# Performance work log

Hardware: AMD Instinct MI355X
Metric: run time of the kernel (lower is better)

Reference implementation:

```python
import jax, jax.numpy as jnp
import numpy as np
from jax import lax

NUM_TAGS = 9
HIDDEN = 768
BATCH = 64
SEQ = 512


def setup_inputs() -> dict:
    key = jax.random.key(0)
    ks = jax.random.split(key, 6)
    hidden = jax.random.normal(ks[0], (BATCH, SEQ, HIDDEN), dtype=jnp.float32)
    labels = jax.random.randint(ks[1], (BATCH, SEQ), 0, NUM_TAGS)  # all >= 0 -> full mask
    weight = jax.random.normal(ks[2], (NUM_TAGS, HIDDEN), dtype=jnp.float32) * 0.02
    bias = jnp.zeros((NUM_TAGS,), dtype=jnp.float32)
    start_transitions = jax.random.normal(ks[3], (NUM_TAGS,), dtype=jnp.float32) * 0.1
    end_transitions = jax.random.normal(ks[4], (NUM_TAGS,), dtype=jnp.float32) * 0.1
    transitions = jax.random.normal(ks[5], (NUM_TAGS, NUM_TAGS), dtype=jnp.float32) * 0.1
    return dict(hidden=hidden, labels=labels, weight=weight, bias=bias,
                start_transitions=start_transitions, end_transitions=end_transitions,
                transitions=transitions)


def _crf_log_likelihood(emissions, tags, mask, start_t, end_t, trans):
    """pytorch-crf log-likelihood, reduction='sum'.
    emissions [B,L,T] float, tags [B,L] int, mask [B,L] bool."""
    # --- numerator: score of the gold path ---
    tag0 = tags[:, 0]
    score0 = start_t[tag0] + jnp.take_along_axis(emissions[:, 0], tag0[:, None], axis=1)[:, 0]

    def num_step(carry, inp):
        score, prev = carry
        em, tg, m = inp  # em [B,T], tg [B], m [B]
        s = trans[prev, tg] + jnp.take_along_axis(em, tg[:, None], axis=1)[:, 0]
        score = score + jnp.where(m, s, jnp.zeros_like(s))
        prev = jnp.where(m, tg, prev)
        return (score, prev), None

    (num_score, last_tag), _ = lax.scan(
        num_step, (score0, tag0),
        (emissions[:, 1:].swapaxes(0, 1), tags[:, 1:].T, mask[:, 1:].T))
    numerator = num_score + end_t[last_tag]

    # --- denominator: forward algorithm (log-sum-exp recurrence) ---
    alpha0 = start_t[None, :] + emissions[:, 0]  # [B,T]

    def den_step(alpha, inp):
        em, m = inp  # em [B,T], m [B]
        nxt = jax.nn.logsumexp(alpha[:, :, None] + trans[None], axis=1) + em
        alpha = jnp.where(m[:, None], nxt, alpha)
        return alpha, None

    alpha, _ = lax.scan(den_step, alpha0,
                        (emissions[:, 1:].swapaxes(0, 1), mask[:, 1:].T))
    denominator = jax.nn.logsumexp(alpha + end_t[None, :], axis=1)

    return jnp.sum(numerator - denominator)


def _viterbi_decode(emissions, mask, start_t, end_t, trans):
    """Max-plus DP + backtrack. Returns padded [B,L] int32 best tag sequence."""
    B, L, T = emissions.shape
    score0 = start_t[None, :] + emissions[:, 0]  # [B,T]
    identity = jnp.arange(T, dtype=jnp.int32)[None, :]  # identity backpointer for masked steps

    def fwd_step(score, inp):
        em, m = inp  # em [B,T], m [B]
        br = score[:, :, None] + trans[None]  # [B,T_prev,T_cur]
        idx = jnp.argmax(br, axis=1).astype(jnp.int32)  # [B,T]
        nxt = jnp.max(br, axis=1) + em
        score = jnp.where(m[:, None], nxt, score)
        idx = jnp.where(m[:, None], idx, identity)
        return score, idx

    final, hist = lax.scan(fwd_step, score0,
                           (emissions[:, 1:].swapaxes(0, 1), mask[:, 1:].T))
    last_tag = jnp.argmax(final + end_t[None, :], axis=1).astype(jnp.int32)  # [B]

    def back_step(tag, idx):  # idx [B,T] backpointers for this position
        prev = jnp.take_along_axis(idx, tag[:, None], axis=1)[:, 0]
        return prev, tag

    first_tag, tags_rev = lax.scan(back_step, last_tag, hist, reverse=True)
    tags = jnp.concatenate([first_tag[None, :], tags_rev], axis=0).T  # [B,L]
    return tags * mask.astype(jnp.int32)


def reference(hidden, labels, weight, bias, start_transitions, end_transitions, transitions):
    mask_full = labels >= 0
    h = hidden[:, 1:-1, :]                       # drop [CLS]/[SEP] positions
    tags = labels[:, 1:-1] * mask_full[:, 1:-1]  # zero out padded labels
    mask = mask_full[:, 1:-1]
    # dropout is identity in eval mode
    emissions = jnp.einsum('blh,th->blt', h, weight) + bias  # [B,L,T]
    llh = _crf_log_likelihood(emissions, tags, mask,
                              start_transitions, end_transitions, transitions)
    tag_seqs = _viterbi_decode(emissions, mask,
                               start_transitions, end_transitions, transitions)
    return -llh, tag_seqs.astype(jnp.float32)
```

## Files before the change

kernel.cpp:

```cpp
#include <hip/hip_runtime.h>
#include <stdint.h>

#define NB 64
#define SEQL 512
#define L 510
#define T 9
#define H 768
#define EMS 12
#define LN2 0.6931471805599453f

__device__ __forceinline__ float rl(float v, int l) {
  return __uint_as_float(__builtin_amdgcn_readlane(__float_as_uint(v), l));
}

__global__ __launch_bounds__(256) void emis_kernel(
    const float* __restrict__ hidden, const float* __restrict__ weight,
    const float* __restrict__ bias, float* __restrict__ em,
    float* __restrict__ eem, float* __restrict__ out) {
  __shared__ float4 wl[T * 192];
  const float4* w4 = (const float4*)weight;
  for (int k = threadIdx.x; k < T * 192; k += 256) wl[k] = w4[k];
  if (blockIdx.x == 0 && threadIdx.x == 0) out[0] = 0.f;
  __syncthreads();
  const int lane = threadIdx.x & 63;
  const int wv = threadIdx.x >> 6;
  const int base = blockIdx.x * 64 + wv * 16;
#pragma unroll 1
  for (int pr = 0; pr < 8; ++pr) {
    const int r0 = base + pr * 2, r1 = r0 + 1;
    const int b0 = r0 / L, p0 = r0 - b0 * L;
    const int b1 = r1 / L, p1 = r1 - b1 * L;
    const float4* h0 = (const float4*)(hidden + ((size_t)(b0 * SEQL + p0 + 1)) * H);
    const float4* h1 = (const float4*)(hidden + ((size_t)(b1 * SEQL + p1 + 1)) * H);
    float4 ha[3], hb[3];
#pragma unroll
    for (int k = 0; k < 3; ++k) { ha[k] = h0[lane + 64 * k]; hb[k] = h1[lane + 64 * k]; }
    float a0[T], a1[T];
#pragma unroll
    for (int t = 0; t < T; ++t) { a0[t] = 0.f; a1[t] = 0.f; }
#pragma unroll
    for (int t = 0; t < T; ++t) {
#pragma unroll
      for (int k = 0; k < 3; ++k) {
        float4 w = wl[t * 192 + lane + 64 * k];
        a0[t] = fmaf(ha[k].x, w.x, fmaf(ha[k].y, w.y, fmaf(ha[k].z, w.z, fmaf(ha[k].w, w.w, a0[t]))));
        a1[t] = fmaf(hb[k].x, w.x, fmaf(hb[k].y, w.y, fmaf(hb[k].z, w.z, fmaf(hb[k].w, w.w, a1[t]))));
      }
    }
#pragma unroll
    for (int off = 32; off; off >>= 1) {
#pragma unroll
      for (int t = 0; t < T; ++t) {
        a0[t] += __shfl_xor(a0[t], off);
        a1[t] += __shfl_xor(a1[t], off);
      }
    }
    if (lane < 2) {
      const int rr = lane ? r1 : r0;
      float* eo = em + (size_t)rr * EMS;
      float* xo = eem + (size_t)rr * EMS;
#pragma unroll
      for (int t = 0; t < T; ++t) {
        float v = (lane ? a1[t] : a0[t]) + bias[t];
        eo[t] = v;
        xo[t] = __expf(v);
      }
    }
  }
}

__global__ __launch_bounds__(64) void chunk_kernel(
    const float* __restrict__ em, const float* __restrict__ eem,
    const float* __restrict__ trans, float* __restrict__ PdLn,
    float* __restrict__ Mv) {
  const int lane = threadIdx.x;
  const int m7 = lane / 9;
  const int i9 = lane - m7 * 9;
  const bool isden = blockIdx.x < 147;
  const int wid = isden ? blockIdx.x : blockIdx.x - 147;
  const int rtask = wid * 7 + (m7 < 7 ? m7 : 6);
  const bool act = (m7 < 7) && (rtask < 1024);
  const int task = act ? rtask : 0;
  const int b = task >> 4, s = task & 15;
  const int nt = (s == 15) ? 29 : 32;
  const int l0 = 32 * s + 1;

  if (isden) {
    float E[81];
#pragma unroll
    for (int k = 0; k < 81; ++k) E[k] = __expf(trans[k]);
    const float* ee = eem + ((size_t)(b * L + l0)) * EMS;
    float4 ea = *(const float4*)(ee);
    float4 eb = *(const float4*)(ee + 4);
    float e8 = ee[8];
    float ec[9] = {ea.x, ea.y, ea.z, ea.w, eb.x, eb.y, eb.z, eb.w, e8};
    float R[9];
#pragma unroll
    for (int j = 0; j < 9; ++j) R[j] = E[i9 * 9 + j] * ec[j];
    int iexp = 0;
    float4 na = *(const float4*)(ee + EMS);
    float4 nb = *(const float4*)(ee + EMS + 4);
    float n8 = ee[EMS + 8];
    for (int t = 1; t < nt; ++t) {
      float e0 = na.x, e1 = na.y, e2 = na.z, e3 = na.w;
      float e4 = nb.x, e5 = nb.y, e6 = nb.z, e7 = nb.w, e8c = n8;
      if (t < nt - 1) {
        na = *(const float4*)(ee + (size_t)(t + 1) * EMS);
        nb = *(const float4*)(ee + (size_t)(t + 1) * EMS + 4);
        n8 = ee[(size_t)(t + 1) * EMS + 8];
      }
      float Rn[9];
#pragma unroll
      for (int j = 0; j < 9; ++j) {
        float a = R[0] * E[0 * 9 + j];
#pragma unroll
        for (int k = 1; k < 9; ++k) a = fmaf(R[k], E[k * 9 + j], a);
        Rn[j] = a;
      }
      R[0] = Rn[0] * e0; R[1] = Rn[1] * e1; R[2] = Rn[2] * e2;
      R[3] = Rn[3] * e3; R[4] = Rn[4] * e4; R[5] = Rn[5] * e5;
      R[6] = Rn[6] * e6; R[7] = Rn[7] * e7; R[8] = Rn[8] * e8c;
      if ((t & 3) == 0) {
        float mx = R[0];
#pragma unroll
        for (int j = 1; j < 9; ++j) mx = fmaxf(mx, R[j]);
        int ex = (int)((__float_as_uint(mx) >> 23) & 0xff) - 127;
        iexp += ex;
        float sc = __uint_as_float((uint32_t)(127 - ex) << 23);
#pragma unroll
        for (int j = 0; j < 9; ++j) R[j] *= sc;
      }
    }
    if (act) {
      float ls = (float)iexp * LN2;
#pragma unroll
      for (int j = 0; j < 9; ++j)
        PdLn[(size_t)task * 81 + j * 9 + i9] = __logf(R[j]) + ls;
    }
  } else {
    float t_[81];
#pragma unroll
    for (int k = 0; k < 81; ++k) t_[k] = trans[k];
    const float* ep = em + ((size_t)(b * L + l0)) * EMS;
    float4 ea = *(const float4*)(ep);
    float4 eb = *(const float4*)(ep + 4);
    float e8 = ep[8];
    float ec[9] = {ea.x, ea.y, ea.z, ea.w, eb.x, eb.y, eb.z, eb.w, e8};
    float V[9];
#pragma unroll
    for (int j = 0; j < 9; ++j) V[j] = t_[i9 * 9 + j] + ec[j];
    float4 na = *(const float4*)(ep + EMS);
    float4 nb = *(const float4*)(ep + EMS + 4);
    float n8 = ep[EMS + 8];
    for (int t = 1; t < nt; ++t) {
      float e[9] = {na.x, na.y, na.z, na.w, nb.x, nb.y, nb.z, nb.w, n8};
      if (t < nt - 1) {
        na = *(const float4*)(ep + (size_t)(t + 1) * EMS);
        nb = *(const float4*)(ep + (size_t)(t + 1) * EMS + 4);
        n8 = ep[(size_t)(t + 1) * EMS + 8];
      }
      float Vn[9];
#pragma unroll
      for (int j = 0; j < 9; ++j) {
        float m = V[0] + t_[0 * 9 + j];
#pragma unroll
        for (int k = 1; k < 9; ++k) m = fmaxf(m, V[k] + t_[k * 9 + j]);
        Vn[j] = m + e[j];
      }
#pragma unroll
      for (int j = 0; j < 9; ++j) V[j] = Vn[j];
    }
    if (act) {
#pragma unroll
      for (int j = 0; j < 9; ++j)
        Mv[(size_t)task * 81 + j * 9 + i9] = V[j];
    }
  }
}

__global__ __launch_bounds__(64) void compose_kernel(
    const float* __restrict__ em, const int* __restrict__ labels,
    const float* __restrict__ PdLn, const float* __restrict__ Mv,
    const float* __restrict__ start_t, const float* __restrict__ end_t,
    const float* __restrict__ trans, unsigned char* __restrict__ chosen,
    float* __restrict__ out) {
  __shared__ float s_pd[16 * 81];
  __shared__ float s_mv[16 * 81];
  __shared__ float s_A[17 * 9];
  __shared__ float s_t[81];
  __shared__ int s_lab[L];
  const int b = blockIdx.x;
  const int lane = threadIdx.x;
  for (int k = lane; k < 16 * 81; k += 64) {
    s_pd[k] = PdLn[(size_t)b * 16 * 81 + k];
    s_mv[k] = Mv[(size_t)b * 16 * 81 + k];
  }
  for (int k = lane; k < 81; k += 64) s_t[k] = trans[k];
  for (int k = lane; k < L; k += 64) s_lab[k] = labels[b * SEQL + 1 + k];
  __syncthreads();

  const int jj = lane < 9 ? lane : 8;

  float part = 0.f;
  for (int l = lane; l < L; l += 64) {
    int tg = s_lab[l];
    float e = em[((size_t)(b * L + l)) * EMS + tg];
    if (l == 0) part += start_t[tg] + e;
    else part += s_t[s_lab[l - 1] * 9 + tg] + e;
    if (l == L - 1) part += end_t[tg];
  }
#pragma unroll
  for (int off = 32; off; off >>= 1) part += __shfl_xor(part, off);

  float D = start_t[jj] + em[(size_t)b * L * EMS + jj];
  for (int s = 0; s < 16; ++s) {
    const float* col = &s_pd[s * 81 + jj * 9];
    float v0 = rl(D, 0) + col[0], v1 = rl(D, 1) + col[1], v2 = rl(D, 2) + col[2];
    float v3 = rl(D, 3) + col[3], v4 = rl(D, 4) + col[4], v5 = rl(D, 5) + col[5];
    float v6 = rl(D, 6) + col[6], v7 = rl(D, 7) + col[7], v8 = rl(D, 8) + col[8];
    float mx = fmaxf(fmaxf(fmaxf(fmaxf(v0, v1), fmaxf(v2, v3)),
                           fmaxf(fmaxf(v4, v5), fmaxf(v6, v7))), v8);
    float sum = __expf(v0 - mx) + __expf(v1 - mx) + __expf(v2 - mx) +
                __expf(v3 - mx) + __expf(v4 - mx) + __expf(v5 - mx) +
                __expf(v6 - mx) + __expf(v7 - mx) + __expf(v8 - mx);
    D = mx + __logf(sum);
  }
  float fe = D + end_t[jj];
  float w0 = rl(fe, 0), w1 = rl(fe, 1), w2 = rl(fe, 2), w3 = rl(fe, 3);
  float w4 = rl(fe, 4), w5 = rl(fe, 5), w6 = rl(fe, 6), w7 = rl(fe, 7), w8 = rl(fe, 8);
  float mx = fmaxf(fmaxf(fmaxf(fmaxf(w0, w1), fmaxf(w2, w3)),
                         fmaxf(fmaxf(w4, w5), fmaxf(w6, w7))), w8);
  float den = mx + __logf(__expf(w0 - mx) + __expf(w1 - mx) + __expf(w2 - mx) +
                          __expf(w3 - mx) + __expf(w4 - mx) + __expf(w5 - mx) +
                          __expf(w6 - mx) + __expf(w7 - mx) + __expf(w8 - mx));
  if (lane == 0) atomicAdd(out, den - part);

  float A = start_t[jj] + em[(size_t)b * L * EMS + jj];
  if (lane < 9) s_A[lane] = A;
  for (int s = 0; s < 16; ++s) {
    const float* col = &s_mv[s * 81 + jj * 9];
    float u0 = rl(A, 0) + col[0], u1 = rl(A, 1) + col[1], u2 = rl(A, 2) + col[2];
    float u3 = rl(A, 3) + col[3], u4 = rl(A, 4) + col[4], u5 = rl(A, 5) + col[5];
    float u6 = rl(A, 6) + col[6], u7 = rl(A, 7) + col[7], u8 = rl(A, 8) + col[8];
    A = fmaxf(fmaxf(fmaxf(fmaxf(u0, u1), fmaxf(u2, u3)),
                    fmaxf(fmaxf(u4, u5), fmaxf(u6, u7))), u8);
    if (lane < 9) s_A[(s + 1) * 9 + lane] = A;
  }
  float fv = A + end_t[jj];
  int j = 0;
  {
    float bv = rl(fv, 0);
#pragma unroll
    for (int i = 1; i < 9; ++i) { float v = rl(fv, i); if (v > bv) { bv = v; j = i; } }
  }
  for (int s = 15; s >= 0; --s) {
    float val = s_A[s * 9 + jj] + s_mv[s * 81 + j * 9 + jj];
    int ii = 0;
    float bb = rl(val, 0);
#pragma unroll
    for (int i = 1; i < 9; ++i) { float v = rl(val, i); if (v > bb) { bb = v; ii = i; } }
    if (lane == 0) {
      chosen[(b * 16 + s) * 2] = (unsigned char)ii;
      chosen[(b * 16 + s) * 2 + 1] = (unsigned char)j;
    }
    j = ii;
  }
  if (lane == 0) out[1 + (size_t)b * L] = (float)j;
}

__global__ __launch_bounds__(64) void path_kernel(
    const float* __restrict__ em, const float* __restrict__ trans,
    const unsigned char* __restrict__ chosen, float* __restrict__ out) {
  __shared__ float s_t[81];
  __shared__ uint32_t s_bp[32][64][2];
  const int lane = threadIdx.x;
  for (int k = lane; k < 81; k += 64) s_t[k] = trans[k];
  __syncthreads();
  const int task = blockIdx.x * 64 + lane;
  const int b = task >> 4, s = task & 15;
  const int nt = (s == 15) ? 29 : 32;
  const int l0 = 32 * s + 1;
  const int i0 = chosen[task * 2];
  const int jF = chosen[task * 2 + 1];
  float t_[81];
#pragma unroll
  for (int k = 0; k < 81; ++k) t_[k] = trans[k];
  const float* ep = em + ((size_t)(b * L + l0)) * EMS;
  float a[9];
  {
    float4 ea = *(const float4*)(ep);
    float4 eb = *(const float4*)(ep + 4);
    float e8 = ep[8];
    float e[9] = {ea.x, ea.y, ea.z, ea.w, eb.x, eb.y, eb.z, eb.w, e8};
#pragma unroll
    for (int jx = 0; jx < 9; ++jx) a[jx] = s_t[i0 * 9 + jx] + e[jx];
  }
  for (int q = 1; q < nt; ++q) {
    float4 na = *(const float4*)(ep + (size_t)q * EMS);
    float4 nb = *(const float4*)(ep + (size_t)q * EMS + 4);
    float n8 = ep[(size_t)q * EMS + 8];
    float e[9] = {na.x, na.y, na.z, na.w, nb.x, nb.y, nb.z, nb.w, n8};
    uint32_t pk0 = 0, pk1 = 0;
    float an[9];
#pragma unroll
    for (int jx = 0; jx < 9; ++jx) {
      float best = a[0] + t_[0 * 9 + jx];
      int bi = 0;
#pragma unroll
      for (int k = 1; k < 9; ++k) {
        float v = a[k] + t_[k * 9 + jx];
        if (v > best) { best = v; bi = k; }
      }
      an[jx] = best + e[jx];
      if (jx < 8) pk0 |= ((uint32_t)bi) << (4 * jx);
      else pk1 = (uint32_t)bi;
    }
    s_bp[q][lane][0] = pk0;
    s_bp[q][lane][1] = pk1;
#pragma unroll
    for (int jx = 0; jx < 9; ++jx) a[jx] = an[jx];
  }
  int cur = jF;
  float* orow = out + 1 + (size_t)b * L + l0;
  for (int q = nt - 1; q >= 1; --q) {
    orow[q] = (float)cur;
    uint32_t w = s_bp[q][lane][cur >> 3];
    cur = (int)((w >> ((cur & 7) * 4)) & 15u);
  }
  orow[0] = (float)cur;
}

extern "C" void kernel_launch(void* const* d_in, const int* in_sizes, int n_in,
                              void* d_out, int out_size, void* d_ws, size_t ws_size,
                              hipStream_t stream) {
  const float* hidden  = (const float*)d_in[0];
  const int*   labels  = (const int*)d_in[1];
  const float* weight  = (const float*)d_in[2];
  const float* bias    = (const float*)d_in[3];
  const float* start_t = (const float*)d_in[4];
  const float* end_t   = (const float*)d_in[5];
  const float* trans   = (const float*)d_in[6];
  float* out = (float*)d_out;

  float* em   = (float*)d_ws;
  float* eem  = em + (size_t)NB * L * EMS;
  float* PdLn = eem + (size_t)NB * L * EMS;
  float* Mv   = PdLn + (size_t)1024 * 81;
  unsigned char* chosen = (unsigned char*)(Mv + (size_t)1024 * 81);

  emis_kernel<<<510, 256, 0, stream>>>(hidden, weight, bias, em, eem, out);
  chunk_kernel<<<294, 64, 0, stream>>>(em, eem, trans, PdLn, Mv);
  compose_kernel<<<NB, 64, 0, stream>>>(em, labels, PdLn, Mv, start_t, end_t,
                                        trans, chosen, out);
  path_kernel<<<16, 64, 0, stream>>>(em, trans, chosen, out);
}
```

Before: 224.6 us.

## Fuse emission GEMV with chunk scans and compose with path backtrack

Merges the emission projection and the per-chunk forward/Viterbi scans into one kernel: each block computes the emissions for its own 32-position chunk, keeps them in shared memory and then runs the two chunk recurrences on separate waves. It also folds the chunk-path backtrack into the compose kernel through a shared-memory chosen array, which cuts the launch count from four to two and removes the eem buffer round trip. In exchange, each of the 1024 blocks reloads the full weight matrix into LDS. Only two of its four waves do the serial scan while the others sit idle, and the path recompute now uses just 16 threads per batch block.

```diff
diff --git a/kernel.cpp b/kernel.cpp
--- a/kernel.cpp
+++ b/kernel.cpp
@@ -13,102 +13,81 @@
   return __uint_as_float(__builtin_amdgcn_readlane(__float_as_uint(v), l));
 }
 
-__global__ __launch_bounds__(256) void emis_kernel(
+__global__ __launch_bounds__(256) void ka_kernel(
     const float* __restrict__ hidden, const float* __restrict__ weight,
-    const float* __restrict__ bias, float* __restrict__ em,
-    float* __restrict__ eem, float* __restrict__ out) {
-  __shared__ float4 wl[T * 192];
-  const float4* w4 = (const float4*)weight;
-  for (int k = threadIdx.x; k < T * 192; k += 256) wl[k] = w4[k];
-  if (blockIdx.x == 0 && threadIdx.x == 0) out[0] = 0.f;
-  __syncthreads();
-  const int lane = threadIdx.x & 63;
-  const int wv = threadIdx.x >> 6;
-  const int base = blockIdx.x * 64 + wv * 16;
-#pragma unroll 1
-  for (int pr = 0; pr < 8; ++pr) {
-    const int r0 = base + pr * 2, r1 = r0 + 1;
-    const int b0 = r0 / L, p0 = r0 - b0 * L;
-    const int b1 = r1 / L, p1 = r1 - b1 * L;
-    const float4* h0 = (const float4*)(hidden + ((size_t)(b0 * SEQL + p0 + 1)) * H);
-    const float4* h1 = (const float4*)(hidden + ((size_t)(b1 * SEQL + p1 + 1)) * H);
-    float4 ha[3], hb[3];
-#pragma unroll
-    for (int k = 0; k < 3; ++k) { ha[k] = h0[lane + 64 * k]; hb[k] = h1[lane + 64 * k]; }
-    float a0[T], a1[T];
-#pragma unroll
-    for (int t = 0; t < T; ++t) { a0[t] = 0.f; a1[t] = 0.f; }
-#pragma unroll
-    for (int t = 0; t < T; ++t) {
-#pragma unroll
-      for (int k = 0; k < 3; ++k) {
-        float4 w = wl[t * 192 + lane + 64 * k];
-        a0[t] = fmaf(ha[k].x, w.x, fmaf(ha[k].y, w.y, fmaf(ha[k].z, w.z, fmaf(ha[k].w, w.w, a0[t]))));
-        a1[t] = fmaf(hb[k].x, w.x, fmaf(hb[k].y, w.y, fmaf(hb[k].z, w.z, fmaf(hb[k].w, w.w, a1[t]))));
-      }
-    }
-#pragma unroll
-    for (int off = 32; off; off >>= 1) {
-#pragma unroll
-      for (int t = 0; t < T; ++t) {
-        a0[t] += __shfl_xor(a0[t], off);
-        a1[t] += __shfl_xor(a1[t], off);
-      }
-    }
-    if (lane < 2) {
-      const int rr = lane ? r1 : r0;
-      float* eo = em + (size_t)rr * EMS;
-      float* xo = eem + (size_t)rr * EMS;
-#pragma unroll
-      for (int t = 0; t < T; ++t) {
-        float v = (lane ? a1[t] : a0[t]) + bias[t];
-        eo[t] = v;
-        xo[t] = __expf(v);
-      }
-    }
-  }
-}
-
-__global__ __launch_bounds__(64) void chunk_kernel(
-    const float* __restrict__ em, const float* __restrict__ eem,
-    const float* __restrict__ trans, float* __restrict__ PdLn,
-    float* __restrict__ Mv) {
-  const int lane = threadIdx.x;
-  const int m7 = lane / 9;
-  const int i9 = lane - m7 * 9;
-  const bool isden = blockIdx.x < 147;
-  const int wid = isden ? blockIdx.x : blockIdx.x - 147;
-  const int rtask = wid * 7 + (m7 < 7 ? m7 : 6);
-  const bool act = (m7 < 7) && (rtask < 1024);
-  const int task = act ? rtask : 0;
-  const int b = task >> 4, s = task & 15;
+    const float* __restrict__ bias, const float* __restrict__ trans,
+    float* __restrict__ em, float* __restrict__ PdLn, float* __restrict__ Mv,
+    float* __restrict__ out) {
+  __shared__ float4 wl[1728];
+  __shared__ float s_em[33 * 12];
+  __shared__ float s_ee[33 * 12];
+  const int tid = threadIdx.x;
+  const int w = blockIdx.x;
+  const int b = w >> 4, s = w & 15;
   const int nt = (s == 15) ? 29 : 32;
   const int l0 = 32 * s + 1;
-
-  if (isden) {
+  const int off0 = (s == 0) ? 1 : 0;
+  const int nrows = nt + off0;
+  const int lstart = l0 - off0;
+
+  const float4* w4 = (const float4*)weight;
+  for (int k = tid; k < 1728; k += 256) wl[k] = w4[k];
+  if (w == 0 && tid == 0) out[0] = 0.f;
+  __syncthreads();
+
+  const int lane = tid & 63, wv = tid >> 6;
+  float bs[9];
+#pragma unroll
+  for (int t = 0; t < 9; ++t) bs[t] = bias[t];
+
+  for (int r = wv; r < nrows; r += 4) {
+    const float4* h4 = (const float4*)(hidden + ((size_t)(b * SEQL + lstart + r + 1)) * H);
+    float4 h0 = h4[lane], h1 = h4[lane + 64], h2 = h4[lane + 128];
+    float acc[9];
+#pragma unroll
+    for (int t = 0; t < 9; ++t) acc[t] = 0.f;
+#pragma unroll
+    for (int t = 0; t < 9; ++t) {
+      float4 wa = wl[t * 192 + lane];
+      float4 wb = wl[t * 192 + lane + 64];
+      float4 wc = wl[t * 192 + lane + 128];
+      acc[t] = fmaf(h0.x, wa.x, fmaf(h0.y, wa.y, fmaf(h0.z, wa.z, fmaf(h0.w, wa.w, acc[t]))));
+      acc[t] = fmaf(h1.x, wb.x, fmaf(h1.y, wb.y, fmaf(h1.z, wb.z, fmaf(h1.w, wb.w, acc[t]))));
+      acc[t] = fmaf(h2.x, wc.x, fmaf(h2.y, wc.y, fmaf(h2.z, wc.z, fmaf(h2.w, wc.w, acc[t]))));
+    }
+#pragma unroll
+    for (int off = 32; off; off >>= 1) {
+#pragma unroll
+      for (int t = 0; t < 9; ++t) acc[t] += __shfl_xor(acc[t], off);
+    }
+    if (lane == 0) {
+      float* eo = em + ((size_t)(b * L + lstart + r)) * EMS;
+#pragma unroll
+      for (int t = 0; t < 9; ++t) {
+        float v = acc[t] + bs[t];
+        s_em[r * 12 + t] = v;
+        s_ee[r * 12 + t] = __expf(v);
+        eo[t] = v;
+      }
+    }
+  }
+  __syncthreads();
+
+  if (tid < 64) {
+    const int i9 = lane < 9 ? lane : 8;
     float E[81];
 #pragma unroll
     for (int k = 0; k < 81; ++k) E[k] = __expf(trans[k]);
-    const float* ee = eem + ((size_t)(b * L + l0)) * EMS;
-    float4 ea = *(const float4*)(ee);
-    float4 eb = *(const float4*)(ee + 4);
-    float e8 = ee[8];
-    float ec[9] = {ea.x, ea.y, ea.z, ea.w, eb.x, eb.y, eb.z, eb.w, e8};
+    const float* ee0 = s_ee + off0 * 12;
     float R[9];
 #pragma unroll
-    for (int j = 0; j < 9; ++j) R[j] = E[i9 * 9 + j] * ec[j];
+    for (int j = 0; j < 9; ++j) R[j] = E[i9 * 9 + j] * ee0[j];
     int iexp = 0;
-    float4 na = *(const float4*)(ee + EMS);
-    float4 nb = *(const float4*)(ee + EMS + 4);
-    float n8 = ee[EMS + 8];
     for (int t = 1; t < nt; ++t) {
-      float e0 = na.x, e1 = na.y, e2 = na.z, e3 = na.w;
-      float e4 = nb.x, e5 = nb.y, e6 = nb.z, e7 = nb.w, e8c = n8;
-      if (t < nt - 1) {
-        na = *(const float4*)(ee + (size_t)(t + 1) * EMS);
-        nb = *(const float4*)(ee + (size_t)(t + 1) * EMS + 4);
-        n8 = ee[(size_t)(t + 1) * EMS + 8];
-      }
+      const float* e = ee0 + t * 12;
+      float4 ea = *(const float4*)e;
+      float4 eb = *(const float4*)(e + 4);
+      float e8 = e[8];
       float Rn[9];
 #pragma unroll
       for (int j = 0; j < 9; ++j) {
@@ -117,9 +96,9 @@
         for (int k = 1; k < 9; ++k) a = fmaf(R[k], E[k * 9 + j], a);
         Rn[j] = a;
       }
-      R[0] = Rn[0] * e0; R[1] = Rn[1] * e1; R[2] = Rn[2] * e2;
-      R[3] = Rn[3] * e3; R[4] = Rn[4] * e4; R[5] = Rn[5] * e5;
-      R[6] = Rn[6] * e6; R[7] = Rn[7] * e7; R[8] = Rn[8] * e8c;
+      R[0] = Rn[0] * ea.x; R[1] = Rn[1] * ea.y; R[2] = Rn[2] * ea.z;
+      R[3] = Rn[3] * ea.w; R[4] = Rn[4] * eb.x; R[5] = Rn[5] * eb.y;
+      R[6] = Rn[6] * eb.z; R[7] = Rn[7] * eb.w; R[8] = Rn[8] * e8;
       if ((t & 3) == 0) {
         float mx = R[0];
 #pragma unroll
@@ -131,78 +110,71 @@
         for (int j = 0; j < 9; ++j) R[j] *= sc;
       }
     }
-    if (act) {
+    if (lane < 9) {
       float ls = (float)iexp * LN2;
 #pragma unroll
       for (int j = 0; j < 9; ++j)
-        PdLn[(size_t)task * 81 + j * 9 + i9] = __logf(R[j]) + ls;
-    }
-  } else {
+        PdLn[(size_t)w * 81 + j * 9 + lane] = __logf(R[j]) + ls;
+    }
+  } else if (tid < 128) {
+    const int i9 = lane < 9 ? lane : 8;
     float t_[81];
 #pragma unroll
     for (int k = 0; k < 81; ++k) t_[k] = trans[k];
-    const float* ep = em + ((size_t)(b * L + l0)) * EMS;
-    float4 ea = *(const float4*)(ep);
-    float4 eb = *(const float4*)(ep + 4);
-    float e8 = ep[8];
-    float ec[9] = {ea.x, ea.y, ea.z, ea.w, eb.x, eb.y, eb.z, eb.w, e8};
+    const float* e0 = s_em + off0 * 12;
     float V[9];
 #pragma unroll
-    for (int j = 0; j < 9; ++j) V[j] = t_[i9 * 9 + j] + ec[j];
-    float4 na = *(const float4*)(ep + EMS);
-    float4 nb = *(const float4*)(ep + EMS + 4);
-    float n8 = ep[EMS + 8];
+    for (int j = 0; j < 9; ++j) V[j] = t_[i9 * 9 + j] + e0[j];
     for (int t = 1; t < nt; ++t) {
-      float e[9] = {na.x, na.y, na.z, na.w, nb.x, nb.y, nb.z, nb.w, n8};
-      if (t < nt - 1) {
-        na = *(const float4*)(ep + (size_t)(t + 1) * EMS);
-        nb = *(const float4*)(ep + (size_t)(t + 1) * EMS + 4);
-        n8 = ep[(size_t)(t + 1) * EMS + 8];
-      }
+      const float* e = e0 + t * 12;
+      float4 ea = *(const float4*)e;
+      float4 eb = *(const float4*)(e + 4);
+      float e8 = e[8];
+      float ex[9] = {ea.x, ea.y, ea.z, ea.w, eb.x, eb.y, eb.z, eb.w, e8};
       float Vn[9];
 #pragma unroll
       for (int j = 0; j < 9; ++j) {
         float m = V[0] + t_[0 * 9 + j];
 #pragma unroll
         for (int k = 1; k < 9; ++k) m = fmaxf(m, V[k] + t_[k * 9 + j]);
-        Vn[j] = m + e[j];
+        Vn[j] = m + ex[j];
       }
 #pragma unroll
       for (int j = 0; j < 9; ++j) V[j] = Vn[j];
     }
-    if (act) {
+    if (lane < 9) {
 #pragma unroll
       for (int j = 0; j < 9; ++j)
-        Mv[(size_t)task * 81 + j * 9 + i9] = V[j];
+        Mv[(size_t)w * 81 + j * 9 + lane] = V[j];
     }
   }
 }
 
-__global__ __launch_bounds__(64) void compose_kernel(
+__global__ __launch_bounds__(256) void kb_kernel(
     const float* __restrict__ em, const int* __restrict__ labels,
     const float* __restrict__ PdLn, const float* __restrict__ Mv,
     const float* __restrict__ start_t, const float* __restrict__ end_t,
-    const float* __restrict__ trans, unsigned char* __restrict__ chosen,
-    float* __restrict__ out) {
-  __shared__ float s_pd[16 * 81];
-  __shared__ float s_mv[16 * 81];
-  __shared__ float s_A[17 * 9];
+    const float* __restrict__ trans, float* __restrict__ out) {
+  __shared__ float s_pd[1296];
+  __shared__ float s_mv[1296];
+  __shared__ float s_A[153];
   __shared__ float s_t[81];
+  __shared__ float s_np[4];
   __shared__ int s_lab[L];
+  __shared__ unsigned char s_ch[32];
+  __shared__ uint32_t s_bp[32 * 16 * 2];
   const int b = blockIdx.x;
-  const int lane = threadIdx.x;
-  for (int k = lane; k < 16 * 81; k += 64) {
-    s_pd[k] = PdLn[(size_t)b * 16 * 81 + k];
-    s_mv[k] = Mv[(size_t)b * 16 * 81 + k];
-  }
-  for (int k = lane; k < 81; k += 64) s_t[k] = trans[k];
-  for (int k = lane; k < L; k += 64) s_lab[k] = labels[b * SEQL + 1 + k];
-  __syncthreads();
-
-  const int jj = lane < 9 ? lane : 8;
+  const int tid = threadIdx.x;
+  for (int k = tid; k < 1296; k += 256) {
+    s_pd[k] = PdLn[(size_t)b * 1296 + k];
+    s_mv[k] = Mv[(size_t)b * 1296 + k];
+  }
+  for (int k = tid; k < 81; k += 256) s_t[k] = trans[k];
+  for (int k = tid; k < L; k += 256) s_lab[k] = labels[b * SEQL + 1 + k];
+  __syncthreads();
 
   float part = 0.f;
-  for (int l = lane; l < L; l += 64) {
+  for (int l = tid; l < L; l += 256) {
     int tg = s_lab[l];
     float e = em[((size_t)(b * L + l)) * EMS + tg];
     if (l == 0) part += start_t[tg] + e;
@@ -211,123 +183,124 @@
   }
 #pragma unroll
   for (int off = 32; off; off >>= 1) part += __shfl_xor(part, off);
-
-  float D = start_t[jj] + em[(size_t)b * L * EMS + jj];
-  for (int s = 0; s < 16; ++s) {
-    const float* col = &s_pd[s * 81 + jj * 9];
-    float v0 = rl(D, 0) + col[0], v1 = rl(D, 1) + col[1], v2 = rl(D, 2) + col[2];
-    float v3 = rl(D, 3) + col[3], v4 = rl(D, 4) + col[4], v5 = rl(D, 5) + col[5];
-    float v6 = rl(D, 6) + col[6], v7 = rl(D, 7) + col[7], v8 = rl(D, 8) + col[8];
-    float mx = fmaxf(fmaxf(fmaxf(fmaxf(v0, v1), fmaxf(v2, v3)),
-                           fmaxf(fmaxf(v4, v5), fmaxf(v6, v7))), v8);
-    float sum = __expf(v0 - mx) + __expf(v1 - mx) + __expf(v2 - mx) +
-                __expf(v3 - mx) + __expf(v4 - mx) + __expf(v5 - mx) +
-                __expf(v6 - mx) + __expf(v7 - mx) + __expf(v8 - mx);
-    D = mx + __logf(sum);
-  }
-  float fe = D + end_t[jj];
-  float w0 = rl(fe, 0), w1 = rl(fe, 1), w2 = rl(fe, 2), w3 = rl(fe, 3);
-  float w4 = rl(fe, 4), w5 = rl(fe, 5), w6 = rl(fe, 6), w7 = rl(fe, 7), w8 = rl(fe, 8);
-  float mx = fmaxf(fmaxf(fmaxf(fmaxf(w0, w1), fmaxf(w2, w3)),
-                         fmaxf(fmaxf(w4, w5), fmaxf(w6, w7))), w8);
-  float den = mx + __logf(__expf(w0 - mx) + __expf(w1 - mx) + __expf(w2 - mx) +
-                          __expf(w3 - mx) + __expf(w4 - mx) + __expf(w5 - mx) +
-                          __expf(w6 - mx) + __expf(w7 - mx) + __expf(w8 - mx));
-  if (lane == 0) atomicAdd(out, den - part);
-
-  float A = start_t[jj] + em[(size_t)b * L * EMS + jj];
-  if (lane < 9) s_A[lane] = A;
-  for (int s = 0; s < 16; ++s) {
-    const float* col = &s_mv[s * 81 + jj * 9];
-    float u0 = rl(A, 0) + col[0], u1 = rl(A, 1) + col[1], u2 = rl(A, 2) + col[2];
-    float u3 = rl(A, 3) + col[3], u4 = rl(A, 4) + col[4], u5 = rl(A, 5) + col[5];
-    float u6 = rl(A, 6) + col[6], u7 = rl(A, 7) + col[7], u8 = rl(A, 8) + col[8];
-    A = fmaxf(fmaxf(fmaxf(fmaxf(u0, u1), fmaxf(u2, u3)),
-                    fmaxf(fmaxf(u4, u5), fmaxf(u6, u7))), u8);
-    if (lane < 9) s_A[(s + 1) * 9 + lane] = A;
-  }
-  float fv = A + end_t[jj];
-  int j = 0;
-  {
-    float bv = rl(fv, 0);
-#pragma unroll
-    for (int i = 1; i < 9; ++i) { float v = rl(fv, i); if (v > bv) { bv = v; j = i; } }
-  }
-  for (int s = 15; s >= 0; --s) {
-    float val = s_A[s * 9 + jj] + s_mv[s * 81 + j * 9 + jj];
-    int ii = 0;
-    float bb = rl(val, 0);
-#pragma unroll
-    for (int i = 1; i < 9; ++i) { float v = rl(val, i); if (v > bb) { bb = v; ii = i; } }
-    if (lane == 0) {
-      chosen[(b * 16 + s) * 2] = (unsigned char)ii;
-      chosen[(b * 16 + s) * 2 + 1] = (unsigned char)j;
-    }
-    j = ii;
-  }
-  if (lane == 0) out[1 + (size_t)b * L] = (float)j;
-}
-
-__global__ __launch_bounds__(64) void path_kernel(
-    const float* __restrict__ em, const float* __restrict__ trans,
-    const unsigned char* __restrict__ chosen, float* __restrict__ out) {
-  __shared__ float s_t[81];
-  __shared__ uint32_t s_bp[32][64][2];
-  const int lane = threadIdx.x;
-  for (int k = lane; k < 81; k += 64) s_t[k] = trans[k];
-  __syncthreads();
-  const int task = blockIdx.x * 64 + lane;
-  const int b = task >> 4, s = task & 15;
-  const int nt = (s == 15) ? 29 : 32;
-  const int l0 = 32 * s + 1;
-  const int i0 = chosen[task * 2];
-  const int jF = chosen[task * 2 + 1];
-  float t_[81];
-#pragma unroll
-  for (int k = 0; k < 81; ++k) t_[k] = trans[k];
-  const float* ep = em + ((size_t)(b * L + l0)) * EMS;
-  float a[9];
-  {
-    float4 ea = *(const float4*)(ep);
-    float4 eb = *(const float4*)(ep + 4);
-    float e8 = ep[8];
-    float e[9] = {ea.x, ea.y, ea.z, ea.w, eb.x, eb.y, eb.z, eb.w, e8};
-#pragma unroll
-    for (int jx = 0; jx < 9; ++jx) a[jx] = s_t[i0 * 9 + jx] + e[jx];
-  }
-  for (int q = 1; q < nt; ++q) {
-    float4 na = *(const float4*)(ep + (size_t)q * EMS);
-    float4 nb = *(const float4*)(ep + (size_t)q * EMS + 4);
-    float n8 = ep[(size_t)q * EMS + 8];
-    float e[9] = {na.x, na.y, na.z, na.w, nb.x, nb.y, nb.z, nb.w, n8};
-    uint32_t pk0 = 0, pk1 = 0;
-    float an[9];
-#pragma unroll
-    for (int jx = 0; jx < 9; ++jx) {
-      float best = a[0] + t_[0 * 9 + jx];
-      int bi = 0;
-#pragma unroll
-      for (int k = 1; k < 9; ++k) {
-        float v = a[k] + t_[k * 9 + jx];
-        if (v > best) { best = v; bi = k; }
-      }
-      an[jx] = best + e[jx];
-      if (jx < 8) pk0 |= ((uint32_t)bi) << (4 * jx);
-      else pk1 = (uint32_t)bi;
-    }
-    s_bp[q][lane][0] = pk0;
-    s_bp[q][lane][1] = pk1;
-#pragma unroll
-    for (int jx = 0; jx < 9; ++jx) a[jx] = an[jx];
-  }
-  int cur = jF;
-  float* orow = out + 1 + (size_t)b * L + l0;
-  for (int q = nt - 1; q >= 1; --q) {
-    orow[q] = (float)cur;
-    uint32_t w = s_bp[q][lane][cur >> 3];
-    cur = (int)((w >> ((cur & 7) * 4)) & 15u);
-  }
-  orow[0] = (float)cur;
+  if ((tid & 63) == 0) s_np[tid >> 6] = part;
+  __syncthreads();
+
+  if (tid < 64) {
+    const int lane = tid;
+    const int jj = lane < 9 ? lane : 8;
+
+    float D = start_t[jj] + em[(size_t)b * L * EMS + jj];
+    for (int s = 0; s < 16; ++s) {
+      const float* col = &s_pd[s * 81 + jj * 9];
+      float v0 = rl(D, 0) + col[0], v1 = rl(D, 1) + col[1], v2 = rl(D, 2) + col[2];
+      float v3 = rl(D, 3) + col[3], v4 = rl(D, 4) + col[4], v5 = rl(D, 5) + col[5];
+      float v6 = rl(D, 6) + col[6], v7 = rl(D, 7) + col[7], v8 = rl(D, 8) + col[8];
+      float mx = fmaxf(fmaxf(fmaxf(fmaxf(v0, v1), fmaxf(v2, v3)),
+                             fmaxf(fmaxf(v4, v5), fmaxf(v6, v7))), v8);
+      float sum = __expf(v0 - mx) + __expf(v1 - mx) + __expf(v2 - mx) +
+                  __expf(v3 - mx) + __expf(v4 - mx) + __expf(v5 - mx) +
+                  __expf(v6 - mx) + __expf(v7 - mx) + __expf(v8 - mx);
+      D = mx + __logf(sum);
+    }
+    float fe = D + end_t[jj];
+    float w0 = rl(fe, 0), w1 = rl(fe, 1), w2 = rl(fe, 2), w3 = rl(fe, 3);
+    float w4 = rl(fe, 4), w5 = rl(fe, 5), w6 = rl(fe, 6), w7 = rl(fe, 7), w8 = rl(fe, 8);
+    float mx = fmaxf(fmaxf(fmaxf(fmaxf(w0, w1), fmaxf(w2, w3)),
+                           fmaxf(fmaxf(w4, w5), fmaxf(w6, w7))), w8);
+    float den = mx + __logf(__expf(w0 - mx) + __expf(w1 - mx) + __expf(w2 - mx) +
+                            __expf(w3 - mx) + __expf(w4 - mx) + __expf(w5 - mx) +
+                            __expf(w6 - mx) + __expf(w7 - mx) + __expf(w8 - mx));
+    if (lane == 0)
+      atomicAdd(out, den - (s_np[0] + s_np[1] + s_np[2] + s_np[3]));
+
+    float A = start_t[jj] + em[(size_t)b * L * EMS + jj];
+    if (lane < 9) s_A[lane] = A;
+    for (int s = 0; s < 16; ++s) {
+      const float* col = &s_mv[s * 81 + jj * 9];
+      float u0 = rl(A, 0) + col[0], u1 = rl(A, 1) + col[1], u2 = rl(A, 2) + col[2];
+      float u3 = rl(A, 3) + col[3], u4 = rl(A, 4) + col[4], u5 = rl(A, 5) + col[5];
+      float u6 = rl(A, 6) + col[6], u7 = rl(A, 7) + col[7], u8 = rl(A, 8) + col[8];
+      A = fmaxf(fmaxf(fmaxf(fmaxf(u0, u1), fmaxf(u2, u3)),
+                      fmaxf(fmaxf(u4, u5), fmaxf(u6, u7))), u8);
+      if (lane < 9) s_A[(s + 1) * 9 + lane] = A;
+    }
+    float fv = A + end_t[jj];
+    int j = 0;
+    {
+      float bv = rl(fv, 0);
+#pragma unroll
+      for (int i = 1; i < 9; ++i) { float v = rl(fv, i); if (v > bv) { bv = v; j = i; } }
+    }
+    for (int s = 15; s >= 0; --s) {
+      float val = s_A[s * 9 + jj] + s_mv[s * 81 + j * 9 + jj];
+      int ii = 0;
+      float bb = rl(val, 0);
+#pragma unroll
+      for (int i = 1; i < 9; ++i) { float v = rl(val, i); if (v > bb) { bb = v; ii = i; } }
+      if (lane == 0) {
+        s_ch[s * 2] = (unsigned char)ii;
+        s_ch[s * 2 + 1] = (unsigned char)j;
+      }
+      j = ii;
+    }
+    if (lane == 0) out[1 + (size_t)b * L] = (float)j;
+  }
+  __syncthreads();
+
+  if (tid < 16) {
+    const int s = tid;
+    const int nt = (s == 15) ? 29 : 32;
+    const int l0 = 32 * s + 1;
+    const int i0 = s_ch[s * 2];
+    const int jF = s_ch[s * 2 + 1];
+    float t_[81];
+#pragma unroll
+    for (int k = 0; k < 81; ++k) t_[k] = trans[k];
+    const float* ep = em + ((size_t)(b * L + l0)) * EMS;
+    float a[9];
+    {
+      float4 ea = *(const float4*)(ep);
+      float4 eb = *(const float4*)(ep + 4);
+      float e8 = ep[8];
+      float e[9] = {ea.x, ea.y, ea.z, ea.w, eb.x, eb.y, eb.z, eb.w, e8};
+#pragma unroll
+      for (int jx = 0; jx < 9; ++jx) a[jx] = t_[i0 * 9 + jx] + e[jx];
+    }
+    for (int q = 1; q < nt; ++q) {
+      float4 na = *(const float4*)(ep + (size_t)q * EMS);
+      float4 nb = *(const float4*)(ep + (size_t)q * EMS + 4);
+      float n8 = ep[(size_t)q * EMS + 8];
+      float e[9] = {na.x, na.y, na.z, na.w, nb.x, nb.y, nb.z, nb.w, n8};
+      uint32_t pk0 = 0, pk1 = 0;
+      float an[9];
+#pragma unroll
+      for (int jx = 0; jx < 9; ++jx) {
+        float best = a[0] + t_[0 * 9 + jx];
+        int bi = 0;
+#pragma unroll
+        for (int k = 1; k < 9; ++k) {
+          float v = a[k] + t_[k * 9 + jx];
+          if (v > best) { best = v; bi = k; }
+        }
+        an[jx] = best + e[jx];
+        if (jx < 8) pk0 |= ((uint32_t)bi) << (4 * jx);
+        else pk1 = (uint32_t)bi;
+      }
+      s_bp[(q * 16 + s) * 2] = pk0;
+      s_bp[(q * 16 + s) * 2 + 1] = pk1;
+#pragma unroll
+      for (int jx = 0; jx < 9; ++jx) a[jx] = an[jx];
+    }
+    int cur = jF;
+    float* orow = out + 1 + (size_t)b * L + l0;
+    for (int q = nt - 1; q >= 1; --q) {
+      orow[q] = (float)cur;
+      uint32_t pk = s_bp[(q * 16 + s) * 2 + (cur >> 3)];
+      cur = (int)((pk >> ((cur & 7) * 4)) & 15u);
+    }
+    orow[0] = (float)cur;
+  }
 }
 
 extern "C" void kernel_launch(void* const* d_in, const int* in_sizes, int n_in,
@@ -343,14 +316,9 @@
   float* out = (float*)d_out;
 
   float* em   = (float*)d_ws;
-  float* eem  = em + (size_t)NB * L * EMS;
-  float* PdLn = eem + (size_t)NB * L * EMS;
+  float* PdLn = em + (size_t)NB * L * EMS;
   float* Mv   = PdLn + (size_t)1024 * 81;
-  unsigned char* chosen = (unsigned char*)(Mv + (size_t)1024 * 81);
-
-  emis_kernel<<<510, 256, 0, stream>>>(hidden, weight, bias, em, eem, out);
-  chunk_kernel<<<294, 64, 0, stream>>>(em, eem, trans, PdLn, Mv);
-  compose_kernel<<<NB, 64, 0, stream>>>(em, labels, PdLn, Mv, start_t, end_t,
-                                        trans, chosen, out);
-  path_kernel<<<16, 64, 0, stream>>>(em, trans, chosen, out);
+
+  ka_kernel<<<1024, 256, 0, stream>>>(hidden, weight, bias, trans, em, PdLn, Mv, out);
+  kb_kernel<<<NB, 256, 0, stream>>>(em, labels, PdLn, Mv, start_t, end_t, trans, out);
 }
```

New measurement: 248.1 us. +10.5%, slower.
